# Performance work log

Hardware: AMD Instinct MI355X
Metric: run time of the kernel (lower is better)

## Reference

```python
import jax, jax.numpy as jnp
import numpy as np

N_GRAPHS = 64
NODES_PER_GRAPH = 1024
N_NODES = N_GRAPHS * NODES_PER_GRAPH
AVG_DEGREE = 32
N_EDGES = N_NODES * AVG_DEGREE
D_FEAT = 256
ALPHA = 0.5
RATIO = 0.5
K = max(int(RATIO * NODES_PER_GRAPH), 1)  # 512 kept nodes per graph


def setup_inputs() -> dict:
    key = jax.random.key(0)
    ks = jax.random.split(key, 6)
    x = jax.random.normal(ks[0], (N_NODES, D_FEAT), dtype=jnp.float32)
    # intra-graph random edges (src, dst local in [0, n), offset by graph id)
    epg = N_EDGES // N_GRAPHS
    src_loc = jax.random.randint(ks[1], (N_EDGES,), 0, NODES_PER_GRAPH, dtype=jnp.int32)
    dst_loc = jax.random.randint(ks[2], (N_EDGES,), 0, NODES_PER_GRAPH, dtype=jnp.int32)
    off = (jnp.arange(N_EDGES, dtype=jnp.int32) // epg) * NODES_PER_GRAPH
    edge_index = jnp.stack([src_loc + off, dst_loc + off])  # [2, E] int32
    batch = jnp.repeat(jnp.arange(N_GRAPHS, dtype=jnp.int32), NODES_PER_GRAPH)
    scale = 1.0 / np.sqrt(D_FEAT)
    w1 = jax.random.normal(ks[3], (D_FEAT, 1), dtype=jnp.float32) * scale
    b1 = jnp.zeros((1,), dtype=jnp.float32)
    wg = jax.random.normal(ks[4], (D_FEAT, 1), dtype=jnp.float32) * scale
    bg = jnp.zeros((1,), dtype=jnp.float32)
    return {"x": x, "edge_index": edge_index, "batch": batch,
            "w1": w1, "b1": b1, "wg": wg, "bg": bg}


def reference(x, edge_index, batch, w1, b1, wg, bg):
    N = x.shape[0]
    row, col = edge_index[0], edge_index[1]
    # remove_self_loops only affects the GCN scoring path
    ew = (row != col).astype(x.dtype)  # zero-weight self loops == removed
    # GCNConv (add_self_loops=False): D^-1/2 A D^-1/2 (X Wg) + bg
    deg = jnp.zeros((N,), x.dtype).at[col].add(ew)
    dis = jnp.where(deg > 0, jax.lax.rsqrt(jnp.maximum(deg, 1.0)), 0.0)
    norm = dis[row] * dis[col] * ew  # [E]
    xw = x @ wg  # [N, 1]
    gcn = jnp.zeros((N, 1), x.dtype).at[col].add(norm[:, None] * xw[row]) + bg
    score = (ALPHA * (x @ w1 + b1) + (1.0 - ALPHA) * gcn).squeeze(-1)  # [N]
    # segmented top-k: equal-sized graphs -> reshape to [B, n]
    sc = score.reshape(N_GRAPHS, NODES_PER_GRAPH)
    _, idx = jax.lax.top_k(sc, K)  # [B, K], descending (matches torch.topk order)
    perm = (idx + (jnp.arange(N_GRAPHS, dtype=idx.dtype) * NODES_PER_GRAPH)[:, None]).reshape(-1)
    x_new = x[perm] * jnp.tanh(score[perm])[:, None]  # [B*K, D]
    batch_new = batch[perm]
    # filter_adj: keep edges with both endpoints selected, relabel by position in perm
    node_map = jnp.full((N,), -1, jnp.int32).at[perm].set(jnp.arange(perm.shape[0], dtype=jnp.int32))
    er, ec = node_map[row], node_map[col]
    valid = (er >= 0) & (ec >= 0)
    new_edge_index = jnp.where(valid[None, :], jnp.stack([er, ec]), -1)  # -1 marks dropped edges
    return x_new, new_edge_index, batch_new
```

## Files before the change

### kernel.cpp

```cpp
#include <hip/hip_runtime.h>

#define NPG 1024
#define NG 64
#define KKEEP 512
#define DF 256
#define NTOT (NG * NPG)
#define NROWS (NG * KKEEP)
#define EPG 32768
#define NB 8
#define EPB (EPG / NB)
#define HI_ROWS 256
#define LO_ROWS (NROWS - HI_ROWS)
#define FXS 1099511627776.0

typedef float vf4 __attribute__((ext_vector_type(4)));
typedef int   vi4 __attribute__((ext_vector_type(4)));

__device__ __forceinline__ unsigned long long cex(unsigned long long a, int t, int k, int j) {
    unsigned long long b = __shfl_xor(a, j, 64);
    bool lower = ((t & j) == 0);
    bool desc  = ((t & k) == 0);
    unsigned long long mn = a < b ? a : b;
    unsigned long long mx = a < b ? b : a;
    return (desc == lower) ? mx : mn;
}

__global__ __launch_bounds__(256) void k_front(const float* __restrict__ x,
                                               const float* __restrict__ w1,
                                               const float* __restrict__ wg,
                                               const int* __restrict__ rows,
                                               const int* __restrict__ cols,
                                               float* __restrict__ sc0,
                                               float* __restrict__ xwg,
                                               int* __restrict__ degp) {
    __shared__ int deg_l[NPG];
    const int b = blockIdx.x;
    const int t = threadIdx.x;
    if (b < NTOT / 4) {
        int node = b * 4 + (t >> 6);
        int lane = t & 63;
        const float4 xv = *reinterpret_cast<const float4*>(x + (size_t)node * DF + lane * 4);
        const float4 av = *reinterpret_cast<const float4*>(w1 + lane * 4);
        const float4 bv = *reinterpret_cast<const float4*>(wg + lane * 4);
        double s1 = (double)xv.x * av.x + (double)xv.y * av.y + (double)xv.z * av.z + (double)xv.w * av.w;
        double s2 = (double)xv.x * bv.x + (double)xv.y * bv.y + (double)xv.z * bv.z + (double)xv.w * bv.w;
#pragma unroll
        for (int off = 32; off; off >>= 1) {
            s1 += __shfl_xor(s1, off);
            s2 += __shfl_xor(s2, off);
        }
        if (lane == 0) { sc0[node] = (float)s1; xwg[node] = (float)s2; }
    } else {
        const int bb = b - NTOT / 4;
        const int g = bb >> 3, sub = bb & 7;
        deg_l[t] = 0; deg_l[t + 256] = 0; deg_l[t + 512] = 0; deg_l[t + 768] = 0;
        __syncthreads();
        const int4* r4 = reinterpret_cast<const int4*>(rows + (size_t)g * EPG + sub * EPB);
        const int4* c4 = reinterpret_cast<const int4*>(cols + (size_t)g * EPG + sub * EPB);
        for (int i = t; i < EPB / 4; i += 256) {
            int4 r = r4[i], c = c4[i];
            if (r.x != c.x) atomicAdd(&deg_l[c.x & (NPG - 1)], 1);
            if (r.y != c.y) atomicAdd(&deg_l[c.y & (NPG - 1)], 1);
            if (r.z != c.z) atomicAdd(&deg_l[c.z & (NPG - 1)], 1);
            if (r.w != c.w) atomicAdd(&deg_l[c.w & (NPG - 1)], 1);
        }
        __syncthreads();
        int* dst = degp + (size_t)bb * NPG;
        dst[t] = deg_l[t]; dst[t + 256] = deg_l[t + 256];
        dst[t + 512] = deg_l[t + 512]; dst[t + 768] = deg_l[t + 768];
    }
}

__global__ __launch_bounds__(1024) void k_gcn(const int* __restrict__ rows,
                                              const int* __restrict__ cols,
                                              const int* __restrict__ degp,
                                              const float* __restrict__ xwg,
                                              unsigned long long* __restrict__ gcnp) {
    __shared__ float dis_l[NPG];
    __shared__ float xwg_l[NPG];
    __shared__ unsigned long long gcn_l[NPG];
    const int t = threadIdx.x;
    const int g = blockIdx.x >> 3, sub = blockIdx.x & 7;
    {
        int d = 0;
#pragma unroll
        for (int p = 0; p < NB; ++p) d += degp[(size_t)(g * NB + p) * NPG + t];
        dis_l[t] = (d > 0) ? (1.0f / sqrtf((float)d)) : 0.0f;
    }
    xwg_l[t] = xwg[g * NPG + t];
    gcn_l[t] = 0;
    __syncthreads();
    const int4* r4 = reinterpret_cast<const int4*>(rows + (size_t)g * EPG + sub * EPB);
    const int4* c4 = reinterpret_cast<const int4*>(cols + (size_t)g * EPG + sub * EPB);
    for (int i = t; i < EPB / 4; i += 1024) {
        int4 r = r4[i], c = c4[i];
        int rl, cl; float term;
        rl = r.x & (NPG - 1); cl = c.x & (NPG - 1);
        if (r.x != c.x) { term = dis_l[rl] * dis_l[cl] * xwg_l[rl];
            atomicAdd(&gcn_l[cl], (unsigned long long)(long long)llrint((double)term * FXS)); }
        rl = r.y & (NPG - 1); cl = c.y & (NPG - 1);
        if (r.y != c.y) { term = dis_l[rl] * dis_l[cl] * xwg_l[rl];
            atomicAdd(&gcn_l[cl], (unsigned long long)(long long)llrint((double)term * FXS)); }
        rl = r.z & (NPG - 1); cl = c.z & (NPG - 1);
        if (r.z != c.z) { term = dis_l[rl] * dis_l[cl] * xwg_l[rl];
            atomicAdd(&gcn_l[cl], (unsigned long long)(long long)llrint((double)term * FXS)); }
        rl = r.w & (NPG - 1); cl = c.w & (NPG - 1);
        if (r.w != c.w) { term = dis_l[rl] * dis_l[cl] * xwg_l[rl];
            atomicAdd(&gcn_l[cl], (unsigned long long)(long long)llrint((double)term * FXS)); }
    }
    __syncthreads();
    gcnp[(size_t)blockIdx.x * NPG + t] = gcn_l[t];
}

__global__ __launch_bounds__(1024) void k_sort(const float* __restrict__ sc0,
                                               const unsigned long long* __restrict__ gcnp,
                                               const float* __restrict__ b1,
                                               const float* __restrict__ bg,
                                               int* __restrict__ node_map,
                                               int2* __restrict__ rowinfo) {
    __shared__ unsigned long long keys[NPG];
    __shared__ float score_l[NPG];
    const int g = blockIdx.x, t = threadIdx.x;
    const int nbase = g * NPG;
    unsigned long long key;
    {
        long long q = 0;
#pragma unroll
        for (int p = 0; p < NB; ++p) q += (long long)gcnp[(size_t)(g * NB + p) * NPG + t];
        float s2 = (float)((double)q * (1.0 / FXS)) + bg[0];
        float s1 = sc0[nbase + t] + b1[0];
        float s = 0.5f * s1 + 0.5f * s2;
        score_l[t] = s;
        unsigned u = __float_as_uint(s);
        u = (u & 0x80000000u) ? ~u : (u | 0x80000000u);
        key = ((unsigned long long)u << 32) | (unsigned long long)(0xFFFFFFFFu - (unsigned)t);
    }
#pragma unroll
    for (int k = 2; k <= 64; k <<= 1)
        for (int j = k >> 1; j > 0; j >>= 1)
            key = cex(key, t, k, j);
    keys[t] = key;
    __syncthreads();
    for (int k = 128; k <= NPG; k <<= 1) {
        for (int j = k >> 1; j >= 64; j >>= 1) {
            int ixj = t ^ j;
            if (ixj > t) {
                unsigned long long a = keys[t], b = keys[ixj];
                bool desc = ((t & k) == 0);
                if (desc ? (a < b) : (a > b)) { keys[t] = b; keys[ixj] = a; }
            }
            __syncthreads();
        }
        key = keys[t];
#pragma unroll
        for (int j = 32; j > 0; j >>= 1)
            key = cex(key, t, k, j);
        if (k < NPG) { keys[t] = key; __syncthreads(); }
    }
    int idx = (int)(0xFFFFFFFFu - (unsigned)(key & 0xFFFFFFFFull)) & (NPG - 1);
    if (t < KKEEP) {
        int row = g * KKEEP + t;
        node_map[nbase + idx] = row;
        rowinfo[row] = make_int2(nbase + idx, __float_as_int(tanhf(score_l[idx])));
    } else {
        node_map[nbase + idx] = -1;
    }
}

__device__ __forceinline__ void edge_block(const int* __restrict__ rows,
                                           const int* __restrict__ cols,
                                           const int* __restrict__ node_map,
                                           float* __restrict__ oute, int E, int eb, int t,
                                           int* map_l) {
    const int g = eb >> 5, sub = eb & 31;
    const int* nm = node_map + g * NPG;
    map_l[t] = nm[t]; map_l[t + 256] = nm[t + 256];
    map_l[t + 512] = nm[t + 512]; map_l[t + 768] = nm[t + 768];
    __syncthreads();
    int i = g * (EPG / 4) + sub * 256 + t;
    vi4 r = __builtin_nontemporal_load(reinterpret_cast<const vi4*>(rows) + i);
    vi4 c = __builtin_nontemporal_load(reinterpret_cast<const vi4*>(cols) + i);
    int ex = map_l[r.x & (NPG - 1)], fx = map_l[c.x & (NPG - 1)];
    int ey = map_l[r.y & (NPG - 1)], fy = map_l[c.y & (NPG - 1)];
    int ez = map_l[r.z & (NPG - 1)], fz = map_l[c.z & (NPG - 1)];
    int ew = map_l[r.w & (NPG - 1)], fw = map_l[c.w & (NPG - 1)];
    vf4 orow, ocol;
    orow.x = (ex >= 0 && fx >= 0) ? (float)ex : -1.0f;  ocol.x = (ex >= 0 && fx >= 0) ? (float)fx : -1.0f;
    orow.y = (ey >= 0 && fy >= 0) ? (float)ey : -1.0f;  ocol.y = (ey >= 0 && fy >= 0) ? (float)fy : -1.0f;
    orow.z = (ez >= 0 && fz >= 0) ? (float)ez : -1.0f;  ocol.z = (ez >= 0 && fz >= 0) ? (float)fz : -1.0f;
    orow.w = (ew >= 0 && fw >= 0) ? (float)ew : -1.0f;  ocol.w = (ew >= 0 && fw >= 0) ? (float)fw : -1.0f;
    __builtin_nontemporal_store(orow, reinterpret_cast<vf4*>(oute) + i);
    __builtin_nontemporal_store(ocol, reinterpret_cast<vf4*>(oute + (size_t)E) + i);
}

__device__ __forceinline__ void gather_row(const float* __restrict__ x, int2 ri, int row,
                                           float* __restrict__ outx, float* __restrict__ outb,
                                           int lane) {
    float tg = __int_as_float(ri.y);
    const float4 v = *reinterpret_cast<const float4*>(x + (size_t)(ri.x & (NTOT - 1)) * DF + lane * 4);
    vf4 o;
    o.x = v.x * tg; o.y = v.y * tg; o.z = v.z * tg; o.w = v.w * tg;
    __builtin_nontemporal_store(o, reinterpret_cast<vf4*>(outx + (size_t)row * DF) + lane);
    if (lane == 0) __builtin_nontemporal_store((float)(row >> 9), outb + row);
}

__global__ __launch_bounds__(256) void k_out(const float* __restrict__ x,
                                             const int* __restrict__ rows,
                                             const int* __restrict__ cols,
                                             const int* __restrict__ node_map,
                                             const int2* __restrict__ rowinfo,
                                             float* __restrict__ outx,
                                             float* __restrict__ oute,
                                             float* __restrict__ outb, int E) {
    __shared__ int map_l[NPG];
    const int b = blockIdx.x, t = threadIdx.x;
    if (b < NROWS / 4) {
        int row = b * 4 + (t >> 6);
        gather_row(x, rowinfo[row], row, outx, outb, t & 63);
    } else {
        edge_block(rows, cols, node_map, oute, E, b - NROWS / 4, t, map_l);
    }
}

__global__ __launch_bounds__(256) void k_edges(const int* __restrict__ rows,
                                               const int* __restrict__ cols,
                                               const int* __restrict__ node_map,
                                               float* __restrict__ oute, int E) {
    __shared__ int map_l[NPG];
    edge_block(rows, cols, node_map, oute, E, blockIdx.x, threadIdx.x, map_l);
}

__global__ __launch_bounds__(256) void k_gather(const float* __restrict__ x,
                                                const int2* __restrict__ rowinfo,
                                                float* __restrict__ outx,
                                                float* __restrict__ outb) {
    int row = blockIdx.x * 4 + (threadIdx.x >> 6);
    gather_row(x, rowinfo[row], row, outx, outb, threadIdx.x & 63);
}

__global__ __launch_bounds__(1024) void k_gather_hi(const float* __restrict__ x,
                                                    const int2* __restrict__ rowinfo,
                                                    float* __restrict__ outx,
                                                    float* __restrict__ outb) {
    __shared__ int2 info[HI_ROWS];
    int tid = threadIdx.x;
    if (tid < HI_ROWS) info[tid] = rowinfo[LO_ROWS + tid];
    __syncthreads();
    for (int it = tid; it < HI_ROWS * 64; it += 1024) {
        int rl = it >> 6, lane = it & 63;
        gather_row(x, info[rl], LO_ROWS + rl, outx, outb, lane);
    }
}

extern "C" void kernel_launch(void* const* d_in, const int* in_sizes, int n_in,
                              void* d_out, int out_size, void* d_ws, size_t ws_size,
                              hipStream_t stream) {
    const float* x = (const float*)d_in[0];
    const int* ei = (const int*)d_in[1];
    const float* w1 = (const float*)d_in[3];
    const float* b1 = (const float*)d_in[4];
    const float* wg = (const float*)d_in[5];
    const float* bg = (const float*)d_in[6];

    const int N = in_sizes[0] / DF;
    const int E = in_sizes[1] / 2;
    const int* rows = ei;
    const int* cols = ei + E;

    float* outx = (float*)d_out;
    float* oute = outx + (size_t)NROWS * DF;
    float* outb = oute + (size_t)2 * E;

    char* sb = (char*)d_out;
    float*              sc0  = (float*)(sb + 0);
    float*              xwg  = (float*)(sb + (1 << 18));
    int*                degp = (int*)(sb + (2 << 18));
    unsigned long long* gcnp = (unsigned long long*)(sb + (10 << 18));

    int tier;
    int*  node_map;
    int2* rowinfo;
    if (ws_size >= (size_t)(NTOT * 4 + NROWS * 8)) {
        tier = 1;
        node_map = (int*)d_ws;
        rowinfo  = (int2*)((char*)d_ws + (size_t)NTOT * 4);
    } else if (ws_size >= (size_t)(NROWS * 8)) {
        tier = 2;
        node_map = (int*)(sb + (26 << 18));
        rowinfo  = (int2*)d_ws;
    } else {
        tier = 3;
        node_map = (int*)(sb + (26 << 18));
        rowinfo  = (int2*)(sb + (size_t)NROWS * DF * 4 - (size_t)NROWS * 8);
    }

    hipLaunchKernelGGL(k_front, dim3(NTOT / 4 + NG * NB), dim3(256), 0, stream,
                       x, w1, wg, rows, cols, sc0, xwg, degp);
    hipLaunchKernelGGL(k_gcn, dim3(NG * NB), dim3(1024), 0, stream, rows, cols, degp, xwg, gcnp);
    hipLaunchKernelGGL(k_sort, dim3(NG), dim3(1024), 0, stream, sc0, gcnp, b1, bg, node_map, rowinfo);
    if (tier == 1) {
        hipLaunchKernelGGL(k_out, dim3(NROWS / 4 + NG * 32), dim3(256), 0, stream,
                           x, rows, cols, node_map, rowinfo, outx, oute, outb, E);
    } else if (tier == 2) {
        hipLaunchKernelGGL(k_edges, dim3(NG * 32), dim3(256), 0, stream, rows, cols, node_map, oute, E);
        hipLaunchKernelGGL(k_gather, dim3(NROWS / 4), dim3(256), 0, stream, x, rowinfo, outx, outb);
    } else {
        hipLaunchKernelGGL(k_edges, dim3(NG * 32), dim3(256), 0, stream, rows, cols, node_map, oute, E);
        hipLaunchKernelGGL(k_gather, dim3(LO_ROWS / 4), dim3(256), 0, stream, x, rowinfo, outx, outb);
        hipLaunchKernelGGL(k_gather_hi, dim3(1), dim3(1024), 0, stream, x, rowinfo, outx, outb);
    }
}
```

Before: 60.90 us.

## Fuse GCN aggregation and per-graph sort using last-block atomic counter

Merges the GCN partial-sum kernel and the per-graph bitonic sort kernel into one launch. Each of the eight sub-blocks of a graph bumps an atomic counter after writing its partials, and the last one to arrive reads all partials and performs the sort. It reuses the gcn_l shared buffer for the sort keys. This removes one kernel launch and its drain gap, at the cost of threadfence overhead and a serialized tail in which only 64 blocks do the sort work.

Measured after the change: 129.5 us. 2.13x slower.

```diff
diff --git a/kernel.cpp b/kernel.cpp
--- a/kernel.cpp
+++ b/kernel.cpp
@@ -32,7 +32,8 @@
                                                const int* __restrict__ cols,
                                                float* __restrict__ sc0,
                                                float* __restrict__ xwg,
-                                               int* __restrict__ degp) {
+                                               int* __restrict__ degp,
+                                               int* __restrict__ cnt) {
     __shared__ int deg_l[NPG];
     const int b = blockIdx.x;
     const int t = threadIdx.x;
@@ -53,6 +54,7 @@
     } else {
         const int bb = b - NTOT / 4;
         const int g = bb >> 3, sub = bb & 7;
+        if (sub == 0 && t == 0) cnt[g] = 0;
         deg_l[t] = 0; deg_l[t + 256] = 0; deg_l[t + 512] = 0; deg_l[t + 768] = 0;
         __syncthreads();
         const int4* r4 = reinterpret_cast<const int4*>(rows + (size_t)g * EPG + sub * EPB);
@@ -71,14 +73,22 @@
     }
 }
 
-__global__ __launch_bounds__(1024) void k_gcn(const int* __restrict__ rows,
-                                              const int* __restrict__ cols,
-                                              const int* __restrict__ degp,
-                                              const float* __restrict__ xwg,
-                                              unsigned long long* __restrict__ gcnp) {
+__global__ __launch_bounds__(1024) void k_gcnsort(const int* __restrict__ rows,
+                                                  const int* __restrict__ cols,
+                                                  const int* __restrict__ degp,
+                                                  const float* __restrict__ xwg,
+                                                  const float* __restrict__ sc0,
+                                                  const float* __restrict__ b1,
+                                                  const float* __restrict__ bg,
+                                                  unsigned long long* __restrict__ gcnp,
+                                                  int* __restrict__ cnt,
+                                                  int* __restrict__ node_map,
+                                                  int2* __restrict__ rowinfo) {
     __shared__ float dis_l[NPG];
     __shared__ float xwg_l[NPG];
     __shared__ unsigned long long gcn_l[NPG];
+    __shared__ float score_l[NPG];
+    __shared__ int is_last;
     const int t = threadIdx.x;
     const int g = blockIdx.x >> 3, sub = blockIdx.x & 7;
     {
@@ -110,17 +120,16 @@
     }
     __syncthreads();
     gcnp[(size_t)blockIdx.x * NPG + t] = gcn_l[t];
-}
-
-__global__ __launch_bounds__(1024) void k_sort(const float* __restrict__ sc0,
-                                               const unsigned long long* __restrict__ gcnp,
-                                               const float* __restrict__ b1,
-                                               const float* __restrict__ bg,
-                                               int* __restrict__ node_map,
-                                               int2* __restrict__ rowinfo) {
-    __shared__ unsigned long long keys[NPG];
-    __shared__ float score_l[NPG];
-    const int g = blockIdx.x, t = threadIdx.x;
+    __syncthreads();
+    if (t == 0) {
+        __threadfence();
+        int old = atomicAdd(&cnt[g], 1);
+        is_last = (old == NB - 1);
+    }
+    __syncthreads();
+    if (!is_last) return;
+    __threadfence();
+
     const int nbase = g * NPG;
     unsigned long long key;
     {
@@ -139,23 +148,23 @@
     for (int k = 2; k <= 64; k <<= 1)
         for (int j = k >> 1; j > 0; j >>= 1)
             key = cex(key, t, k, j);
-    keys[t] = key;
+    gcn_l[t] = key;
     __syncthreads();
     for (int k = 128; k <= NPG; k <<= 1) {
         for (int j = k >> 1; j >= 64; j >>= 1) {
             int ixj = t ^ j;
             if (ixj > t) {
-                unsigned long long a = keys[t], b = keys[ixj];
+                unsigned long long a = gcn_l[t], b = gcn_l[ixj];
                 bool desc = ((t & k) == 0);
-                if (desc ? (a < b) : (a > b)) { keys[t] = b; keys[ixj] = a; }
+                if (desc ? (a < b) : (a > b)) { gcn_l[t] = b; gcn_l[ixj] = a; }
             }
             __syncthreads();
         }
-        key = keys[t];
+        key = gcn_l[t];
 #pragma unroll
         for (int j = 32; j > 0; j >>= 1)
             key = cex(key, t, k, j);
-        if (k < NPG) { keys[t] = key; __syncthreads(); }
+        if (k < NPG) { gcn_l[t] = key; __syncthreads(); }
     }
     int idx = (int)(0xFFFFFFFFu - (unsigned)(key & 0xFFFFFFFFull)) & (NPG - 1);
     if (t < KKEEP) {
@@ -276,6 +285,7 @@
     float*              xwg  = (float*)(sb + (1 << 18));
     int*                degp = (int*)(sb + (2 << 18));
     unsigned long long* gcnp = (unsigned long long*)(sb + (10 << 18));
+    int*                cnt  = (int*)(sb + (27 << 18));
 
     int tier;
     int*  node_map;
@@ -295,9 +305,9 @@
     }
 
     hipLaunchKernelGGL(k_front, dim3(NTOT / 4 + NG * NB), dim3(256), 0, stream,
-                       x, w1, wg, rows, cols, sc0, xwg, degp);
-    hipLaunchKernelGGL(k_gcn, dim3(NG * NB), dim3(1024), 0, stream, rows, cols, degp, xwg, gcnp);
-    hipLaunchKernelGGL(k_sort, dim3(NG), dim3(1024), 0, stream, sc0, gcnp, b1, bg, node_map, rowinfo);
+                       x, w1, wg, rows, cols, sc0, xwg, degp, cnt);
+    hipLaunchKernelGGL(k_gcnsort, dim3(NG * NB), dim3(1024), 0, stream,
+                       rows, cols, degp, xwg, sc0, b1, bg, gcnp, cnt, node_map, rowinfo);
     if (tier == 1) {
         hipLaunchKernelGGL(k_out, dim3(NROWS / 4 + NG * 32), dim3(256), 0, stream,
                            x, rows, cols, node_map, rowinfo, outx, oute, outb, E);
```
